# Performance work log

Hardware: AMD Instinct MI355X
Metric: run time of the kernel (lower is better)

Reference implementation:

```python
import jax, jax.numpy as jnp
import numpy as np


def setup_inputs() -> dict:
    B, Lq, Lk, D, F, H = 2, 2048, 2048, 128, 128, 8
    key = jax.random.key(0)
    ks = jax.random.split(key, 8)
    X_Q = jax.random.normal(ks[0], (B, Lq, D), dtype=jnp.float32)
    X_K = jax.random.normal(ks[1], (B, Lk, D), dtype=jnp.float32)
    X_V = jax.random.normal(ks[2], (B, Lk, F), dtype=jnp.float32)
    mask = jax.random.randint(ks[3], (B, 1, Lq, Lk), 0, 2, dtype=jnp.int32)
    # xavier_normal for [H, D, D]: std = sqrt(2/(D+D))
    W_Q = jax.random.normal(ks[4], (H, D, D), dtype=jnp.float32) * np.sqrt(2.0 / (D + D))
    W_K = jax.random.normal(ks[5], (H, D, D), dtype=jnp.float32) * np.sqrt(2.0 / (D + D))
    W_V = jax.random.normal(ks[6], (H, F, F), dtype=jnp.float32) * np.sqrt(2.0 / (F + F))
    O = jax.random.normal(ks[7], (F * H, F), dtype=jnp.float32) * np.sqrt(2.0 / (F * H + F))
    return {"X_Q": X_Q, "X_K": X_K, "X_V": X_V, "mask": mask,
            "W_Q": W_Q, "W_K": W_K, "W_V": W_V, "O": O}


def reference(X_Q, X_K, X_V, mask, W_Q, W_K, W_V, O):
    B, Lq, D = X_Q.shape
    H = W_Q.shape[0]
    F = W_V.shape[1]
    # torch.einsum with repeated in-operand index ('hdd') takes the diagonal
    dq = jnp.diagonal(W_Q, axis1=1, axis2=2)  # [H, D]
    dk = jnp.diagonal(W_K, axis1=1, axis2=2)  # [H, D]
    dv = jnp.diagonal(W_V, axis1=1, axis2=2)  # [H, F]
    g = dq * dk                               # fused per-head QK diagonal scale [H, D]
    scale = 1.0 / jnp.sqrt(jnp.asarray(D, dtype=X_Q.dtype))
    scores = jnp.einsum('bqd,hd,bkd->bhqk', X_Q, g, X_K) * scale  # [B,H,Lq,Lk]
    scores = jnp.where(mask == 0, jnp.asarray(-jnp.inf, scores.dtype), scores)
    A = jax.nn.softmax(scores, axis=-1)
    # O_h = A @ (diag(dv_h) scaled V)
    Oh = jnp.einsum('bhqk,hf,bkf->bhqf', A, dv, X_V)  # [B,H,Lq,F]
    Oh = Oh.transpose(0, 2, 1, 3).reshape(B, Lq, H * F)
    return jnp.einsum('bqx,xf->bqf', Oh, O)
```

## Files before the change

kernel.cpp:

```cpp
#include <hip/hip_runtime.h>

typedef __bf16 bf16;
typedef __bf16 bf16x4 __attribute__((ext_vector_type(4)));
typedef __bf16 bf16x8 __attribute__((ext_vector_type(8)));
typedef float f32x4 __attribute__((ext_vector_type(4)));
typedef short s16x4 __attribute__((ext_vector_type(4)));
typedef unsigned int u32;
typedef unsigned long long u64;

#define B_ 2
#define H_ 8
#define L_ 2048
#define D_ 128
#define F_ 128
#define QT 128
#define KT 64
#define NKT (L_ / KT)
#define NQT (L_ / QT)

#define WS_KB 0u
#define WS_VT (1u << 20)
#define WS_MB (2u << 20)

#define SMEM_BYTES 136192
#define POX_OFF 32768
#define POX_STRIDE 132
#define SOH_OFF 100352
#define SOH_STRIDE 136
#define SO2_STRIDE 136
#define LWS_OFF 135168

__device__ __forceinline__ void dma16(const void* g, void* l) {
    __builtin_amdgcn_global_load_lds(
        (const __attribute__((address_space(1))) u32*)g,
        (__attribute__((address_space(3))) u32*)l, 16, 0, 0);
}

__device__ __forceinline__ f32x4 mfma32(bf16x8 a, bf16x8 b, f32x4 c) {
    return __builtin_amdgcn_mfma_f32_16x16x32_bf16(a, b, c, 0, 0, 0);
}

__device__ __forceinline__ f32x4 mfma16(bf16x4 a, bf16x4 b, f32x4 c) {
#if __has_builtin(__builtin_amdgcn_mfma_f32_16x16x16_bf16)
    return __builtin_amdgcn_mfma_f32_16x16x16_bf16(a, b, c, 0, 0, 0);
#else
    s16x4 as = __builtin_bit_cast(s16x4, a);
    s16x4 bs = __builtin_bit_cast(s16x4, b);
    return __builtin_amdgcn_mfma_f32_16x16x16bf16_1k(as, bs, c, 0, 0, 0);
#endif
}

__device__ __forceinline__ float fast_exp2(float x) {
#if __has_builtin(__builtin_amdgcn_exp2f)
    return __builtin_amdgcn_exp2f(x);
#else
    return exp2f(x);
#endif
}

__global__ __launch_bounds__(256)
void prep_all(const float* __restrict__ XK, const float* __restrict__ XV,
              const int* __restrict__ mask, bf16* __restrict__ Kb,
              bf16* __restrict__ Vtb, u64* __restrict__ bits)
{
    const int bid = blockIdx.x;
    const int tid = threadIdx.x;
    if (bid < 8192) {
        int wv = bid * 4 + (tid >> 6);
        int lane = tid & 63;
        size_t base = (size_t)wv * 256;
        #pragma unroll
        for (int s = 0; s < 4; ++s) {
            int m = mask[base + s * 64 + lane];
            u64 bal = __ballot(m != 0);
            if (lane == 0) bits[(size_t)wv * 4 + s] = bal;
        }
    } else if (bid < 8448) {
        int gid = (bid - 8192) * 256 + tid;
        int row = gid >> 4;
        int j   = gid & 15;
        const float* src = XK + (size_t)row * 128 + j * 8;
        float4 v0 = *(const float4*)src;
        float4 v1 = *(const float4*)(src + 4);
        bf16x8 w;
        w[0] = (bf16)v0.x; w[1] = (bf16)v0.y; w[2] = (bf16)v0.z; w[3] = (bf16)v0.w;
        w[4] = (bf16)v1.x; w[5] = (bf16)v1.y; w[6] = (bf16)v1.z; w[7] = (bf16)v1.w;
        int jp = j ^ (row & 15);
        *(bf16x8*)(Kb + (size_t)row * 128 + jp * 8) = w;
    } else {
        int tile = bid - 8448;
        int bb = tile >> 5, kt = tile & 31;
        #pragma unroll
        for (int i = 0; i < 4; ++i) {
            int idx  = tid * 4 + i;
            int fblk = idx >> 6;
            int lane = idx & 63;
            int c = lane & 15, quad = lane >> 4;
            int fi = fblk >> 1, kh = fblk & 1;
            int f = fi * 16 + c;
            int kb = kt * 64 + kh * 32 + quad * 4;
            bf16x8 w;
            #pragma unroll
            for (int j = 0; j < 4; ++j) {
                w[j]     = (bf16)XV[(size_t)(bb * L_ + kb + j) * F_ + f];
                w[4 + j] = (bf16)XV[(size_t)(bb * L_ + kb + 16 + j) * F_ + f];
            }
            *(bf16x8*)(Vtb + (size_t)tile * 8192 + fblk * 512 + lane * 8) = w;
        }
    }
}

__global__ __launch_bounds__(512, 2)
void attn_fused_kernel(const float* __restrict__ XQ, const bf16* __restrict__ Kb,
                       const bf16* __restrict__ Vtb, const u64* __restrict__ bits,
                       const float* __restrict__ WQ, const float* __restrict__ WK,
                       const float* __restrict__ WV, const float* __restrict__ Om,
                       float* __restrict__ out)
{
    __shared__ __align__(16) char smem[SMEM_BYTES];
    __shared__ __align__(16) float g_s[128];

    bf16* sK0  = (bf16*)smem;
    bf16* sK1  = (bf16*)(smem + 16384);
    float* pOx = (float*)(smem + POX_OFF);
    bf16* sO2t = (bf16*)(smem + POX_OFF);
    bf16* sOh  = (bf16*)(smem + SOH_OFF);
    float* lws = (float*)(smem + LWS_OFF);

    const int tid  = threadIdx.x;
    const int wave = tid >> 6;
    const int lane = tid & 63;
    const int c    = lane & 15;
    const int quad = lane >> 4;
    const int qt = blockIdx.x, h = blockIdx.y, b = blockIdx.z;
    const int q0 = qt * QT;

    const int kh   = wave >> 2;
    const int msel = wave & 3;
    const int fv  = tid & 127;
    const int grp = tid >> 7;

    if (tid < 128) {
        float wq = WQ[(h * D_ + tid) * D_ + tid];
        float wk = WK[(h * D_ + tid) * D_ + tid];
        g_s[tid] = wq * wk * 0.12752230502179406f;
    }
    __syncthreads();

    const char* gK = (const char*)Kb + (size_t)(b * L_) * 256;
    const char* gV = (const char*)Vtb + (size_t)(b * NKT) * 16384;

    dma16(gK + tid * 16, (char*)sK0 + tid * 16);
    dma16(gK + 8192 + tid * 16, (char*)sK0 + 8192 + tid * 16);

    bf16x8 qfrag[2][4];
    #pragma unroll
    for (int mi = 0; mi < 2; ++mi) {
        const float* qrow = XQ + (size_t)(b * L_ + q0 + msel * 32 + mi * 16 + c) * D_;
        #pragma unroll
        for (int kc = 0; kc < 4; ++kc) {
            int d0 = kc * 32 + quad * 8;
            float4 v0 = *(const float4*)(qrow + d0);
            float4 v1 = *(const float4*)(qrow + d0 + 4);
            float4 g0 = *(const float4*)(g_s + d0);
            float4 g1 = *(const float4*)(g_s + d0 + 4);
            bf16x8 w;
            w[0] = (bf16)(v0.x * g0.x); w[1] = (bf16)(v0.y * g0.y);
            w[2] = (bf16)(v0.z * g0.z); w[3] = (bf16)(v0.w * g0.w);
            w[4] = (bf16)(v1.x * g1.x); w[5] = (bf16)(v1.y * g1.y);
            w[6] = (bf16)(v1.z * g1.z); w[7] = (bf16)(v1.w * g1.w);
            qfrag[mi][kc] = w;
        }
    }

    f32x4 oacc[2][8];
    #pragma unroll
    for (int mi = 0; mi < 2; ++mi)
        #pragma unroll
        for (int fi = 0; fi < 8; ++fi)
            #pragma unroll
            for (int r = 0; r < 4; ++r) oacc[mi][fi][r] = 0.f;
    float lsum[2] = {0.f, 0.f};

    const u64* mrow0 = bits + (size_t)(b * L_ + q0 + msel * 32 + c) * NKT;
    const u64* mrow1 = mrow0 + (size_t)16 * NKT;

    #pragma unroll 2
    for (int kt = 0; kt < NKT; ++kt) {
        bf16* sK  = (kt & 1) ? sK1 : sK0;
        bf16* sKn = (kt & 1) ? sK0 : sK1;

        asm volatile("s_barrier" ::: "memory");

        bf16x8 vload[8];
        {
            const char* gvt = gV + (size_t)kt * 16384 + kh * 1024 + lane * 16;
            #pragma unroll
            for (int fi = 0; fi < 8; ++fi)
                vload[fi] = *(const bf16x8*)(gvt + fi * 2048);
        }
        u64 mb0 = mrow0[kt];
        u64 mb1 = mrow1[kt];

        if (kt + 1 < NKT) {
            const char* gkn = gK + (size_t)(kt + 1) * 16384;
            dma16(gkn + tid * 16, (char*)sKn + tid * 16);
            dma16(gkn + 8192 + tid * 16, (char*)sKn + 8192 + tid * 16);
            asm volatile("s_waitcnt vmcnt(12)" ::: "memory");
        } else {
            asm volatile("s_waitcnt vmcnt(10)" ::: "memory");
        }
        asm volatile("s_barrier" ::: "memory");

        f32x4 tacc[2][2];
        #pragma unroll
        for (int mi = 0; mi < 2; ++mi)
            #pragma unroll
            for (int kti = 0; kti < 2; ++kti)
                #pragma unroll
                for (int r = 0; r < 4; ++r) tacc[mi][kti][r] = 0.f;

        #pragma unroll
        for (int kti = 0; kti < 2; ++kti) {
            const bf16* krow = sK + ((kh * 2 + kti) * 16 + c) * 128;
            #pragma unroll
            for (int kc = 0; kc < 4; ++kc) {
                bf16x8 kfrag = *(const bf16x8*)(krow + (((kc * 4 + quad) ^ c) * 8));
                tacc[0][kti] = mfma32(kfrag, qfrag[0][kc], tacc[0][kti]);
                tacc[1][kti] = mfma32(kfrag, qfrag[1][kc], tacc[1][kti]);
            }
        }

        bf16x4 pfrag[2][2];
        #pragma unroll
        for (int mi = 0; mi < 2; ++mi) {
            u64 mb = mi ? mb1 : mb0;
            #pragma unroll
            for (int kti = 0; kti < 2; ++kti) {
                #pragma unroll
                for (int r = 0; r < 4; ++r) {
                    int pos = kh * 32 + kti * 16 + quad * 4 + r;
                    float p = ((mb >> pos) & 1ull) ? fast_exp2(tacc[mi][kti][r]) : 0.f;
                    lsum[mi] += p;
                    pfrag[mi][kti][r] = (bf16)p;
                }
            }
        }

        #pragma unroll
        for (int fi = 0; fi < 8; ++fi) {
            bf16x4 v0 = __builtin_shufflevector(vload[fi], vload[fi], 0, 1, 2, 3);
            bf16x4 v1 = __builtin_shufflevector(vload[fi], vload[fi], 4, 5, 6, 7);
            #pragma unroll
            for (int mi = 0; mi < 2; ++mi) {
                oacc[mi][fi] = mfma16(pfrag[mi][0], v0, oacc[mi][fi]);
                oacc[mi][fi] = mfma16(pfrag[mi][1], v1, oacc[mi][fi]);
            }
        }
    }

    #pragma unroll
    for (int mi = 0; mi < 2; ++mi) {
        float v = lsum[mi];
        v += __shfl_xor(v, 16); v += __shfl_xor(v, 32);
        if (lane < 16) lws[wave * 32 + mi * 16 + lane] = v;
    }
    if (tid < 128)
        g_s[tid] = WV[(h * F_ + tid) * F_ + tid];
    __syncthreads();

    if (kh == 1) {
        #pragma unroll
        for (int mi = 0; mi < 2; ++mi)
            #pragma unroll
            for (int fi = 0; fi < 8; ++fi)
                #pragma unroll
                for (int r = 0; r < 4; ++r)
                    pOx[(msel * 32 + mi * 16 + quad * 4 + r) * POX_STRIDE + fi * 16 + c]
                        = oacc[mi][fi][r];
    }
    __syncthreads();

    if (kh == 0) {
        #pragma unroll
        for (int mi = 0; mi < 2; ++mi) {
            float linv[4];
            #pragma unroll
            for (int r = 0; r < 4; ++r) {
                int s = mi * 16 + quad * 4 + r;
                linv[r] = 1.0f / (lws[msel * 32 + s] + lws[(4 + msel) * 32 + s]);
            }
            #pragma unroll
            for (int fi = 0; fi < 8; ++fi)
                #pragma unroll
                for (int r = 0; r < 4; ++r) {
                    int row = msel * 32 + mi * 16 + quad * 4 + r;
                    float v = (oacc[mi][fi][r] + pOx[row * POX_STRIDE + fi * 16 + c]) * linv[r];
                    sOh[row * SOH_STRIDE + fi * 16 + c] = (bf16)v;
                }
        }
    }
    __syncthreads();

    #pragma unroll
    for (int i = 0; i < 8; ++i) {
        int fp4 = grp * 32 + i * 4;
        bf16x4 w;
        #pragma unroll
        for (int j = 0; j < 4; ++j) {
            int x = fp4 + j;
            w[j] = (bf16)(Om[(h * F_ + x) * F_ + fv] * g_s[x]);
        }
        *(bf16x4*)(sO2t + fv * SO2_STRIDE + fp4) = w;
    }
    __syncthreads();

    const int pm = wave;
    bf16x8 afr[4];
    const bf16* ohrow = sOh + (pm * 16 + c) * SOH_STRIDE;
    #pragma unroll
    for (int kc = 0; kc < 4; ++kc)
        afr[kc] = *(const bf16x8*)(ohrow + kc * 32 + quad * 8);

    #pragma unroll
    for (int nt = 0; nt < 8; ++nt) {
        f32x4 pacc;
        #pragma unroll
        for (int r = 0; r < 4; ++r) pacc[r] = 0.f;
        const bf16* orow = sO2t + (nt * 16 + c) * SO2_STRIDE;
        #pragma unroll
        for (int kc = 0; kc < 4; ++kc) {
            bf16x8 bfrag = *(const bf16x8*)(orow + kc * 32 + quad * 8);
            pacc = mfma32(afr[kc], bfrag, pacc);
        }
        #pragma unroll
        for (int r = 0; r < 4; ++r) {
            int qg = q0 + pm * 16 + quad * 4 + r;
            atomicAdd(out + ((size_t)(b * L_ + qg) * F_ + nt * 16 + c), pacc[r]);
        }
    }
}

extern "C" void kernel_launch(void* const* d_in, const int* in_sizes, int n_in,
                              void* d_out, int out_size, void* d_ws, size_t ws_size,
                              hipStream_t stream) {
    const float* XQ   = (const float*)d_in[0];
    const float* XK   = (const float*)d_in[1];
    const float* XV   = (const float*)d_in[2];
    const int*   mask = (const int*)d_in[3];
    const float* WQ   = (const float*)d_in[4];
    const float* WK   = (const float*)d_in[5];
    const float* WV   = (const float*)d_in[6];
    const float* Om   = (const float*)d_in[7];
    float* out = (float*)d_out;

    char* ws = (char*)d_ws;
    bf16* Kb   = (bf16*)(ws + WS_KB);
    bf16* Vtb  = (bf16*)(ws + WS_VT);
    u64*  bits = (u64*)(ws + WS_MB);

    prep_all<<<8512, 256, 0, stream>>>(XK, XV, mask, Kb, Vtb, bits);
    hipMemsetAsync(out, 0, (size_t)out_size * sizeof(float), stream);

    dim3 grid(NQT, H_, B_);
    attn_fused_kernel<<<grid, 512, 0, stream>>>(XQ, Kb, Vtb, bits, WQ, WK, WV, Om, out);
}
```

Measured before the change: 180.8 us.

## Stage V tiles through LDS via async DMA and shrink shared memory footprint

V tiles, which each wave used to load directly from global memory into registers, are now double-buffered into LDS with global_load_lds DMA alongside K. The prep kernel writes V in a new XOR-swizzled layout so the LDS reads avoid bank conflicts. To make room, the cross-half oacc reduction is split into two passes over mi, and the pOx/sO2t scratch is reused in the K buffer region, cutting total shared memory from about 136KB to about 72KB. The goal is to drop redundant per-wave global V loads and ease register pressure, at the cost of extra LDS traffic and two more barriers in the epilogue.

```diff
diff --git a/kernel.cpp b/kernel.cpp
--- a/kernel.cpp
+++ b/kernel.cpp
@@ -22,13 +22,12 @@
 #define WS_VT (1u << 20)
 #define WS_MB (2u << 20)
 
-#define SMEM_BYTES 136192
-#define POX_OFF 32768
+#define SMEM_BYTES 72704
 #define POX_STRIDE 132
-#define SOH_OFF 100352
+#define SOH_OFF 36864
 #define SOH_STRIDE 136
 #define SO2_STRIDE 136
-#define LWS_OFF 135168
+#define LWS_OFF 71680
 
 __device__ __forceinline__ void dma16(const void* g, void* l) {
     __builtin_amdgcn_global_load_lds(
@@ -92,20 +91,18 @@
         int bb = tile >> 5, kt = tile & 31;
         #pragma unroll
         for (int i = 0; i < 4; ++i) {
-            int idx  = tid * 4 + i;
-            int fblk = idx >> 6;
-            int lane = idx & 63;
-            int c = lane & 15, quad = lane >> 4;
-            int fi = fblk >> 1, kh = fblk & 1;
-            int f = fi * 16 + c;
+            int idx = tid * 4 + i;
+            int f = idx >> 3, p = idx & 7;
+            int kh = p >> 2, quad = p & 3;
             int kb = kt * 64 + kh * 32 + quad * 4;
+            const float* src = XV + (size_t)(bb * L_ + kb) * F_ + f;
             bf16x8 w;
             #pragma unroll
             for (int j = 0; j < 4; ++j) {
-                w[j]     = (bf16)XV[(size_t)(bb * L_ + kb + j) * F_ + f];
-                w[4 + j] = (bf16)XV[(size_t)(bb * L_ + kb + 16 + j) * F_ + f];
-            }
-            *(bf16x8*)(Vtb + (size_t)tile * 8192 + fblk * 512 + lane * 8) = w;
+                w[j]     = (bf16)src[(size_t)j * F_];
+                w[4 + j] = (bf16)src[(size_t)(16 + j) * F_];
+            }
+            *(bf16x8*)(Vtb + (size_t)tile * 8192 + f * 64 + ((p ^ (f & 7)) * 8)) = w;
         }
     }
 }
@@ -122,8 +119,10 @@
 
     bf16* sK0  = (bf16*)smem;
     bf16* sK1  = (bf16*)(smem + 16384);
-    float* pOx = (float*)(smem + POX_OFF);
-    bf16* sO2t = (bf16*)(smem + POX_OFF);
+    bf16* sV0  = (bf16*)(smem + 32768);
+    bf16* sV1  = (bf16*)(smem + 49152);
+    float* pOx = (float*)smem;
+    bf16* sO2t = (bf16*)smem;
     bf16* sOh  = (bf16*)(smem + SOH_OFF);
     float* lws = (float*)(smem + LWS_OFF);
 
@@ -152,6 +151,8 @@
 
     dma16(gK + tid * 16, (char*)sK0 + tid * 16);
     dma16(gK + 8192 + tid * 16, (char*)sK0 + 8192 + tid * 16);
+    dma16(gV + tid * 16, (char*)sV0 + tid * 16);
+    dma16(gV + 8192 + tid * 16, (char*)sV0 + 8192 + tid * 16);
 
     bf16x8 qfrag[2][4];
     #pragma unroll
@@ -185,30 +186,30 @@
     const u64* mrow0 = bits + (size_t)(b * L_ + q0 + msel * 32 + c) * NKT;
     const u64* mrow1 = mrow0 + (size_t)16 * NKT;
 
+    const int psw = ((kh * 4 + quad) ^ (c & 7)) * 8;
+
     #pragma unroll 2
     for (int kt = 0; kt < NKT; ++kt) {
         bf16* sK  = (kt & 1) ? sK1 : sK0;
+        bf16* sV  = (kt & 1) ? sV1 : sV0;
         bf16* sKn = (kt & 1) ? sK0 : sK1;
+        bf16* sVn = (kt & 1) ? sV0 : sV1;
 
         asm volatile("s_barrier" ::: "memory");
 
-        bf16x8 vload[8];
-        {
-            const char* gvt = gV + (size_t)kt * 16384 + kh * 1024 + lane * 16;
-            #pragma unroll
-            for (int fi = 0; fi < 8; ++fi)
-                vload[fi] = *(const bf16x8*)(gvt + fi * 2048);
-        }
         u64 mb0 = mrow0[kt];
         u64 mb1 = mrow1[kt];
 
         if (kt + 1 < NKT) {
             const char* gkn = gK + (size_t)(kt + 1) * 16384;
+            const char* gvn = gV + (size_t)(kt + 1) * 16384;
             dma16(gkn + tid * 16, (char*)sKn + tid * 16);
             dma16(gkn + 8192 + tid * 16, (char*)sKn + 8192 + tid * 16);
-            asm volatile("s_waitcnt vmcnt(12)" ::: "memory");
+            dma16(gvn + tid * 16, (char*)sVn + tid * 16);
+            dma16(gvn + 8192 + tid * 16, (char*)sVn + 8192 + tid * 16);
+            asm volatile("s_waitcnt vmcnt(6)" ::: "memory");
         } else {
-            asm volatile("s_waitcnt vmcnt(10)" ::: "memory");
+            asm volatile("s_waitcnt vmcnt(2)" ::: "memory");
         }
         asm volatile("s_barrier" ::: "memory");
 
@@ -249,8 +250,9 @@
 
         #pragma unroll
         for (int fi = 0; fi < 8; ++fi) {
-            bf16x4 v0 = __builtin_shufflevector(vload[fi], vload[fi], 0, 1, 2, 3);
-            bf16x4 v1 = __builtin_shufflevector(vload[fi], vload[fi], 4, 5, 6, 7);
+            bf16x8 vp = *(const bf16x8*)(sV + (fi * 16 + c) * 64 + psw);
+            bf16x4 v0 = __builtin_shufflevector(vp, vp, 0, 1, 2, 3);
+            bf16x4 v1 = __builtin_shufflevector(vp, vp, 4, 5, 6, 7);
             #pragma unroll
             for (int mi = 0; mi < 2; ++mi) {
                 oacc[mi][fi] = mfma16(pfrag[mi][0], v0, oacc[mi][fi]);
@@ -269,21 +271,18 @@
         g_s[tid] = WV[(h * F_ + tid) * F_ + tid];
     __syncthreads();
 
-    if (kh == 1) {
-        #pragma unroll
-        for (int mi = 0; mi < 2; ++mi)
+    #pragma unroll
+    for (int mi = 0; mi < 2; ++mi) {
+        if (kh == 1) {
             #pragma unroll
             for (int fi = 0; fi < 8; ++fi)
                 #pragma unroll
                 for (int r = 0; r < 4; ++r)
-                    pOx[(msel * 32 + mi * 16 + quad * 4 + r) * POX_STRIDE + fi * 16 + c]
+                    pOx[(msel * 16 + quad * 4 + r) * POX_STRIDE + fi * 16 + c]
                         = oacc[mi][fi][r];
-    }
-    __syncthreads();
-
-    if (kh == 0) {
-        #pragma unroll
-        for (int mi = 0; mi < 2; ++mi) {
+        }
+        __syncthreads();
+        if (kh == 0) {
             float linv[4];
             #pragma unroll
             for (int r = 0; r < 4; ++r) {
@@ -294,13 +293,14 @@
             for (int fi = 0; fi < 8; ++fi)
                 #pragma unroll
                 for (int r = 0; r < 4; ++r) {
-                    int row = msel * 32 + mi * 16 + quad * 4 + r;
-                    float v = (oacc[mi][fi][r] + pOx[row * POX_STRIDE + fi * 16 + c]) * linv[r];
-                    sOh[row * SOH_STRIDE + fi * 16 + c] = (bf16)v;
+                    int row_c = msel * 16 + quad * 4 + r;
+                    int row_q = msel * 32 + mi * 16 + quad * 4 + r;
+                    float v = (oacc[mi][fi][r] + pOx[row_c * POX_STRIDE + fi * 16 + c]) * linv[r];
+                    sOh[row_q * SOH_STRIDE + fi * 16 + c] = (bf16)v;
                 }
         }
-    }
-    __syncthreads();
+        __syncthreads();
+    }
 
     #pragma unroll
     for (int i = 0; i < 8; ++i) {
```

Result: faster. 176.0 us (-2.6%).
